# Performance work log

Measured on AMD Instinct MI355X. Metric: run time of the kernel, lower is better.

The kernel has to match this reference:

```python
import jax, jax.numpy as jnp
import numpy as np

B, LQ, LKV = 8, 512, 512
D, H, DH, FF = 1024, 16, 64, 4096
CH, CHID = 16, 32  # AttentionBiasMLP channels
EPS_LOG = 1e-6
EPS_LN = 1e-6


def _ln(x, g, b):
    mu = jnp.mean(x, axis=-1, keepdims=True)
    var = jnp.var(x, axis=-1, keepdims=True)
    return (x - mu) * jax.lax.rsqrt(var + EPS_LN) * g + b


def setup_inputs() -> dict:
    key = jax.random.key(0)
    ks = jax.random.split(key, 24)
    s = 0.02
    inp = {
        "q": jax.random.normal(ks[0], (B, LQ, D), jnp.float32),
        "kv": jax.random.normal(ks[1], (B, LKV, D), jnp.float32),
        "attn_map": jax.random.uniform(ks[2], (B, CH, LQ + 1, LKV + 1), jnp.float32),
        # attention projections (torch Linear: y = x @ W.T + b)
        "Wq": jax.random.normal(ks[3], (D, D)) * s, "bq": jnp.zeros((D,)),
        "Wk": jax.random.normal(ks[4], (D, D)) * s, "bk": jnp.zeros((D,)),
        "Wv": jax.random.normal(ks[5], (D, D)) * s, "bv": jnp.zeros((D,)),
        "Wm": jax.random.normal(ks[6], (D, D)) * s, "bm": jnp.zeros((D,)),
        # AttentionBiasMLP 1x1 convs: weight [out_ch, in_ch]
        "Wc1": jax.random.normal(ks[7], (CHID, CH)) * s, "bc1": jnp.zeros((CHID,)),
        "Wc2": jax.random.normal(ks[8], (CH, CHID)) * s, "bc2": jnp.zeros((CH,)),
        # FFN: Linear(D,FF) -> ReLU -> Linear(FF,D)
        "Wf1": jax.random.normal(ks[9], (FF, D)) * s, "bf1": jnp.zeros((FF,)),
        "Wf2": jax.random.normal(ks[10], (D, FF)) * s, "bf2": jnp.zeros((D,)),
        # LayerNorms
        "g1": jnp.ones((D,)), "b1": jnp.zeros((D,)),
        "g2": jnp.ones((D,)), "b2": jnp.zeros((D,)),
    }
    return inp


def _forward(q, kv, attn_map, Wq, bq, Wk, bk, Wv, bv, Wm, bm,
             Wc1, bc1, Wc2, bc2, Wf1, bf1, Wf2, bf2, g1, b1, g2, b2):
    # attention bias: log of cropped attn_map through 1x1-conv MLP with exact GELU
    log_map = jnp.log(attn_map[:, :, 1:, 1:] + EPS_LOG)               # [B,CH,LQ,LKV]
    h = jnp.einsum('bcqk,oc->boqk', log_map, Wc1) + bc1[None, :, None, None]
    h = jax.nn.gelu(h, approximate=False)
    attn_bias = jnp.einsum('bcqk,oc->boqk', h, Wc2) + bc2[None, :, None, None]

    # MHAtt: project, split heads
    qh = (q @ Wq.T + bq).reshape(B, LQ, H, DH).transpose(0, 2, 1, 3)   # [B,H,LQ,DH]
    kh = (kv @ Wk.T + bk).reshape(B, LKV, H, DH).transpose(0, 2, 1, 3)
    vh = (kv @ Wv.T + bv).reshape(B, LKV, H, DH).transpose(0, 2, 1, 3)

    scores = jnp.einsum('bhqd,bhkd->bhqk', qh, kh) / np.sqrt(DH).astype(np.float32)
    scores = scores + attn_bias
    att = jax.nn.softmax(scores, axis=-1)
    ctx = jnp.einsum('bhqk,bhkd->bhqd', att, vh)                       # [B,H,LQ,DH]
    ctx = ctx.transpose(0, 2, 1, 3).reshape(B, LQ, D)
    atted = ctx @ Wm.T + bm

    x = _ln(q + atted, g1, b1)
    ffn = jax.nn.relu(x @ Wf1.T + bf1) @ Wf2.T + bf2
    x = _ln(x + ffn, g2, b2)
    return x


def reference(q, kv, attn_map, Wq, bq, Wk, bk, Wv, bv, Wm, bm,
              Wc1, bc1, Wc2, bc2, Wf1, bf1, Wf2, bf2, g1, b1, g2, b2):
    return _forward(q, kv, attn_map, Wq, bq, Wk, bk, Wv, bv, Wm, bm,
                    Wc1, bc1, Wc2, bc2, Wf1, bf1, Wf2, bf2, g1, b1, g2, b2)
```

## Files before the change

### kernel.cpp

```cpp
#include <hip/hip_runtime.h>
#include <hip/hip_bf16.h>

typedef __bf16 bf16_t;
typedef __bf16 bf16x4_t __attribute__((ext_vector_type(4)));
typedef __bf16 bf16x8_t __attribute__((ext_vector_type(8)));
typedef float  f32x4_t  __attribute__((ext_vector_type(4)));

#define B_   8
#define LQ_  512
#define LKV_ 512
#define D_   1024
#define H_   16
#define DH_  64
#define FF_  4096

__device__ __forceinline__ f32x4_t mfma16(bf16x8_t a, bf16x8_t b, f32x4_t c) {
    return __builtin_amdgcn_mfma_f32_16x16x32_bf16(a, b, c, 0, 0, 0);
}

__device__ __forceinline__ void gload_lds16(const bf16_t* g, bf16_t* l) {
    __builtin_amdgcn_global_load_lds(
        (const __attribute__((address_space(1))) void*)g,
        (__attribute__((address_space(3))) void*)l, 16, 0, 0);
}

__device__ __forceinline__ int xcd_swz(int pid, int nwg) {
    return (pid & 7) * (nwg >> 3) + (pid >> 3);
}

__device__ __forceinline__ float gelu_fast(float h) {
    const float e = exp2f(h * -2.45546696f);
    return h * __builtin_amdgcn_rcpf(1.f + e);
}

__global__ __launch_bounds__(256)
void cvt_all_kernel(const float* __restrict__ q,  const float* __restrict__ kv,
                    const float* __restrict__ Wq, const float* __restrict__ Wk,
                    const float* __restrict__ Wv, const float* __restrict__ Wm,
                    const float* __restrict__ Wf1,const float* __restrict__ Wf2,
                    bf16_t* __restrict__ dq, bf16_t* __restrict__ dW,
                    bf16_t* __restrict__ dF) {
    const int i = blockIdx.x * 256 + threadIdx.x;
    const float* s; bf16_t* d; int j;
    if (i < 1048576)      { s = q;   d = dq;           j = i; }
    else if (i < 2097152) { s = kv;  d = dq + 4194304; j = i - 1048576; }
    else if (i < 2359296) { s = Wq;  d = dW;           j = i - 2097152; }
    else if (i < 2621440) { s = Wk;  d = dW + 1048576; j = i - 2359296; }
    else if (i < 2883584) { s = Wv;  d = dW + 2097152; j = i - 2621440; }
    else if (i < 3145728) { s = Wm;  d = dW + 3145728; j = i - 2883584; }
    else if (i < 4194304) { s = Wf1; d = dF;           j = i - 3145728; }
    else                  { s = Wf2; d = dF + 4194304; j = i - 4194304; }
    const float4 v = ((const float4*)s)[j];
    bf16x4_t o;
    o[0] = (bf16_t)v.x; o[1] = (bf16_t)v.y; o[2] = (bf16_t)v.z; o[3] = (bf16_t)v.w;
    ((bf16x4_t*)d)[j] = o;
}

__global__ __launch_bounds__(256)
void pack3_kernel(const float* __restrict__ a, const float* __restrict__ b,
                  const float* __restrict__ c, float* __restrict__ o) {
    const int i = blockIdx.x * 256 + threadIdx.x;
    o[i] = a[i]; o[1024 + i] = b[i]; o[2048 + i] = c[i];
}

__global__ __launch_bounds__(256)
void bias_mlp_mfma(const float* __restrict__ amap,
                   const float* __restrict__ Wc1, const float* __restrict__ bc1,
                   const float* __restrict__ Wc2, const float* __restrict__ bc2,
                   bf16_t* __restrict__ biasb) {
    __shared__ __align__(16) char lds[4][8192];
    const int t = threadIdx.x, lane = t & 63, w = t >> 6;
    const int l15 = lane & 15, lg = lane >> 4;
    char* Xs = lds[w];
    char* Hs = lds[w] + 3072;

    bf16x8_t b1f[2], b2f;
    f32x4_t bc1v[2];
#pragma unroll
    for (int ot = 0; ot < 2; ot++) {
        bf16x8_t v;
#pragma unroll
        for (int i = 0; i < 8; i++) {
            const int kk = (lg * 8 + i) & 15;
            const float wv = Wc1[(ot * 16 + l15) * 16 + kk] * 0.69314718055994531f;
            v[i] = (lg < 2) ? (bf16_t)wv : (bf16_t)0.f;
        }
        b1f[ot] = v;
        const float bb = bc1[ot * 16 + l15];
        bc1v[ot] = f32x4_t{bb, bb, bb, bb};
    }
    {
        bf16x8_t v;
#pragma unroll
        for (int i = 0; i < 8; i++) v[i] = (bf16_t)Wc2[l15 * 32 + lg * 8 + i];
        b2f = v;
    }
    const float bc2s = bc2[l15];
    const f32x4_t cinit2 = f32x4_t{bc2s, bc2s, bc2s, bc2s};

    const int posb = (blockIdx.x * 4 + w) * 64;
    const int b  = posb >> 18;
    const int q  = (posb >> 9) & 511;
    const int k0 = posb & 511;

    const float* src = amap + (size_t)(b * 16) * 263169 + (size_t)(q + 1) * 513 + (k0 + 1 + lane);
    bf16_t xr[16];
#pragma unroll
    for (int c = 0; c < 16; c++) {
        const float v = src[(size_t)c * 263169];
        xr[c] = (bf16_t)__log2f(v + 1e-6f);
    }
    *(bf16x8_t*)(Xs + lane * 48)      = *(bf16x8_t*)&xr[0];
    *(bf16x8_t*)(Xs + lane * 48 + 16) = *(bf16x8_t*)&xr[8];

    const int lgm16 = (lg & 1) * 16;
    f32x4_t h1[4][2];
#pragma unroll
    for (int p = 0; p < 4; p++) {
        const bf16x8_t a1 = *(const bf16x8_t*)(Xs + (p * 16 + l15) * 48 + lgm16);
#pragma unroll
        for (int ot = 0; ot < 2; ot++)
            h1[p][ot] = mfma16(a1, b1f[ot], bc1v[ot]);
    }

#pragma unroll
    for (int p = 0; p < 4; p++)
#pragma unroll
        for (int ot = 0; ot < 2; ot++)
#pragma unroll
            for (int r = 0; r < 4; r++) {
                const float g = gelu_fast(h1[p][ot][r]);
                *(bf16_t*)(Hs + (p * 16 + lg * 4 + r) * 80 + (ot * 16 + l15) * 2) = (bf16_t)g;
            }

    const size_t obase = ((size_t)(b * 16 + l15) * 512 + q) * 512 + k0;
#pragma unroll
    for (int p = 0; p < 4; p++) {
        const bf16x8_t a2 = *(const bf16x8_t*)(Hs + (p * 16 + l15) * 80 + lg * 16);
        const f32x4_t o2 = mfma16(a2, b2f, cinit2);
        bf16x4_t ov;
#pragma unroll
        for (int r = 0; r < 4; r++) ov[r] = (bf16_t)o2[r];
        *(bf16x4_t*)&biasb[obase + p * 16 + lg * 4] = ov;
    }
}

template <int EPI, bool SPLIT>
__global__ __launch_bounds__(256)
void gemm_bt(const bf16_t* __restrict__ A, const bf16_t* __restrict__ A2,
             const bf16_t* __restrict__ Bw,
             const float* __restrict__ bias, float* __restrict__ Cf,
             bf16_t* __restrict__ Cb, int M, int N, int Klen, int lda) {
    __shared__ __align__(16) bf16_t As[2][128 * 32];
    __shared__ __align__(16) bf16_t Bs[2][128 * 32];
    const int t = threadIdx.x, lane = t & 63, w = t >> 6;
    const int wr = w >> 1, wc = w & 1;
    const int ntn = N >> 7;
    const int nwg = (M >> 7) * ntn;
    const int wg  = xcd_swz((int)blockIdx.x, nwg);
    const int gsz = 8 * ntn;
    const int gid = wg / gsz;
    const int rem = wg - gid * gsz;
    const int tm  = gid * 8 + (rem & 7);
    const int tn  = rem >> 3;
    const int l15 = lane & 15, lg = lane >> 4;
    const int ks = SPLIT ? blockIdx.y : 0;
    const int koff = SPLIT ? ks * Klen : 0;
    if (EPI == 3 && tn >= 8) A = A2;

    const int c0_ = t;
    const int c1_ = t + 256;
    const int r0 = c0_ >> 2, k0 = c0_ & 3;
    const int r1 = c1_ >> 2, k1 = c1_ & 3;
    const int b0 = (w * 64) * 8;
    const int b1 = (256 + w * 64) * 8;
    const bf16_t* Abase0 = A  + (size_t)(tm * 128 + r0) * lda + koff + k0 * 8;
    const bf16_t* Abase1 = A  + (size_t)(tm * 128 + r1) * lda + koff + k1 * 8;
    const bf16_t* Bbase0 = Bw + (size_t)(tn * 128 + r0) * lda + koff + k0 * 8;
    const bf16_t* Bbase1 = Bw + (size_t)(tn * 128 + r1) * lda + koff + k1 * 8;

    f32x4_t acc[4][4];
#pragma unroll
    for (int i = 0; i < 4; i++)
#pragma unroll
        for (int j = 0; j < 4; j++) acc[i][j] = f32x4_t{0.f, 0.f, 0.f, 0.f};

    const int nk = Klen >> 5;

    gload_lds16(Abase0, &As[0][b0]);
    gload_lds16(Abase1, &As[0][b1]);
    gload_lds16(Bbase0, &Bs[0][b0]);
    gload_lds16(Bbase1, &Bs[0][b1]);
    asm volatile("s_waitcnt vmcnt(0)" ::: "memory");
    __syncthreads();

    int cur = 0;
    for (int kt = 0; kt < nk; ++kt) {
        if (kt + 1 < nk) {
            const int ko = (kt + 1) * 32;
            gload_lds16(Abase0 + ko, &As[cur ^ 1][b0]);
            gload_lds16(Abase1 + ko, &As[cur ^ 1][b1]);
            gload_lds16(Bbase0 + ko, &Bs[cur ^ 1][b0]);
            gload_lds16(Bbase1 + ko, &Bs[cur ^ 1][b1]);
        }

        const bf16_t* Ac = As[cur];
        const bf16_t* Bc = Bs[cur];
        bf16x8_t af[4], bfv[4];
#pragma unroll
        for (int mt = 0; mt < 4; mt++)
            af[mt] = *(const bf16x8_t*)&Ac[(wr * 64 + mt * 16 + l15) * 32 + lg * 8];
#pragma unroll
        for (int nt = 0; nt < 4; nt++)
            bfv[nt] = *(const bf16x8_t*)&Bc[(wc * 64 + nt * 16 + l15) * 32 + lg * 8];
#pragma unroll
        for (int mt = 0; mt < 4; mt++)
#pragma unroll
            for (int nt = 0; nt < 4; nt++)
                acc[mt][nt] = mfma16(af[mt], bfv[nt], acc[mt][nt]);

        if (kt + 1 < nk) {
            asm volatile("s_waitcnt vmcnt(0)" ::: "memory");
            __syncthreads();
            cur ^= 1;
        }
    }

#pragma unroll
    for (int nt = 0; nt < 4; nt++) {
        const int col = tn * 128 + wc * 64 + nt * 16 + l15;
        float bv = bias[col];
        if (SPLIT && ks != 0) bv = 0.f;
#pragma unroll
        for (int mt = 0; mt < 4; mt++) {
#pragma unroll
            for (int r = 0; r < 4; r++) {
                const int row = tm * 128 + wr * 64 + mt * 16 + lg * 4 + r;
                float v = acc[mt][nt][r] + bv;
                if (EPI == 2) v = fmaxf(v, 0.f);
                if (EPI == 3 && tn < 8) v *= 0.125f;
                if (EPI == 0) Cf[(size_t)ks * M * N + (size_t)row * N + col] = v;
                else if (EPI == 3)
                    Cb[(size_t)(col >> 10) * 4194304 + (size_t)row * 1024 + (col & 1023)] = (bf16_t)v;
                else Cb[(size_t)row * N + col] = (bf16_t)v;
            }
        }
    }
}

__global__ __launch_bounds__(256)
void attn_kernel(const bf16_t* __restrict__ Qp, const bf16_t* __restrict__ Kp,
                 const bf16_t* __restrict__ Vp, const bf16_t* __restrict__ biasb,
                 bf16_t* __restrict__ ctx) {
    __shared__ __align__(16) bf16_t Qs[64 * 64];
    __shared__ __align__(16) bf16_t Ks[64 * 64];
    __shared__ __align__(16) bf16_t Vts[64 * 64];
    __shared__ __align__(16) bf16_t Ps[64 * 64];
    __shared__ __align__(16) bf16_t Bbs[64 * 64];

    const int bid = xcd_swz((int)blockIdx.x, 1024);
    const int qt = bid & 7, h = (bid >> 3) & 15, b = bid >> 7;
    const int t = threadIdx.x, lane = t & 63, w = t >> 6;
    const int l15 = lane & 15, lg = lane >> 4;

#pragma unroll
    for (int i = 0; i < 2; i++) {
        const int c = t + i * 256;
        const int row = c >> 3, cg = c & 7;
        const uint4 v = *(const uint4*)&Qp[(((size_t)(b * LQ_ + qt * 64 + row)) * H_ + h) * DH_ + cg * 8];
        *(uint4*)((char*)Qs + row * 128 + ((cg ^ (row & 7)) << 4)) = v;
    }

    f32x4_t oacc[4];
#pragma unroll
    for (int i = 0; i < 4; i++) oacc[i] = f32x4_t{0.f, 0.f, 0.f, 0.f};
    float mrow[4] = {-1e30f, -1e30f, -1e30f, -1e30f};
    float lrow[4] = {0.f, 0.f, 0.f, 0.f};

    const bf16_t* bias_tile = biasb + ((size_t)(b * H_ + h) * LQ_ + qt * 64) * LKV_;

    for (int kt = 0; kt < 8; ++kt) {
        __syncthreads();
#pragma unroll
        for (int i = 0; i < 2; i++) {
            const int c = t + i * 256;
            const int row = c >> 3, cg = c & 7;
            const uint4 v = *(const uint4*)&Kp[(((size_t)(b * LKV_ + kt * 64 + row)) * H_ + h) * DH_ + cg * 8];
            *(uint4*)((char*)Ks + row * 128 + ((cg ^ (row & 7)) << 4)) = v;
        }
#pragma unroll
        for (int i = 0; i < 2; i++) {
            const int c = t + i * 256;
            const int row = c >> 3, cg = c & 7;
            const uint4 bv4 = *(const uint4*)&bias_tile[(size_t)row * LKV_ + kt * 64 + cg * 8];
            *(uint4*)&Bbs[row * 64 + cg * 8] = bv4;
        }
#pragma unroll
        for (int i = 0; i < 2; i++) {
            const int c = t + i * 256;
            const int k = c >> 3, dg = c & 7;
            const bf16x8_t vv = *(const bf16x8_t*)&Vp[(((size_t)(b * LKV_ + kt * 64 + k)) * H_ + h) * DH_ + dg * 8];
#pragma unroll
            for (int j = 0; j < 8; j++) {
                const int d = dg * 8 + j;
                *(bf16_t*)((char*)Vts + d * 128 + ((((k * 2) >> 4) ^ (d & 7)) << 4) + ((k * 2) & 15)) = vv[j];
            }
        }
        __syncthreads();

        f32x4_t sacc[4];
#pragma unroll
        for (int i = 0; i < 4; i++) sacc[i] = f32x4_t{0.f, 0.f, 0.f, 0.f};
        bf16x8_t aq[2];
        {
            const int rowq = w * 16 + l15;
#pragma unroll
            for (int kc = 0; kc < 2; kc++)
                aq[kc] = *(const bf16x8_t*)((const char*)Qs + rowq * 128 + (((kc * 4 + lg) ^ (rowq & 7)) << 4));
        }
#pragma unroll
        for (int nt = 0; nt < 4; nt++) {
            const int rowk = nt * 16 + l15;
#pragma unroll
            for (int kc = 0; kc < 2; kc++) {
                const bf16x8_t bk = *(const bf16x8_t*)((const char*)Ks + rowk * 128 + (((kc * 4 + lg) ^ (rowk & 7)) << 4));
                sacc[nt] = mfma16(aq[kc], bk, sacc[nt]);
            }
        }

        float esc[4];
#pragma unroll
        for (int r = 0; r < 4; r++) {
            const int qr = w * 16 + lg * 4 + r;
            float mx = -1e30f;
#pragma unroll
            for (int nt = 0; nt < 4; nt++) {
                const float bvv = (float)Bbs[qr * 64 + nt * 16 + l15];
                const float v = sacc[nt][r] + bvv;
                sacc[nt][r] = v;
                mx = fmaxf(mx, v);
            }
#pragma unroll
            for (int msk = 8; msk >= 1; msk >>= 1) mx = fmaxf(mx, __shfl_xor(mx, msk));
            const float mnew = fmaxf(mrow[r], mx);
            esc[r] = __expf(mrow[r] - mnew);
            mrow[r] = mnew;
            float rs = 0.f;
#pragma unroll
            for (int nt = 0; nt < 4; nt++) {
                const float p = __expf(sacc[nt][r] - mnew);
                sacc[nt][r] = p;
                rs += p;
            }
#pragma unroll
            for (int msk = 8; msk >= 1; msk >>= 1) rs += __shfl_xor(rs, msk);
            lrow[r] = lrow[r] * esc[r] + rs;
        }

#pragma unroll
        for (int r = 0; r < 4; r++) {
            const int prow = w * 16 + lg * 4 + r;
#pragma unroll
            for (int nt = 0; nt < 4; nt++) {
                const int pc2 = (nt * 16 + l15) * 2;
                *(bf16_t*)((char*)Ps + prow * 128 + (((pc2 >> 4) ^ (prow & 7)) << 4) + (pc2 & 15)) =
                    (bf16_t)sacc[nt][r];
            }
        }
        asm volatile("s_waitcnt lgkmcnt(0)" ::: "memory");
        __builtin_amdgcn_sched_barrier(0);

#pragma unroll
        for (int dt = 0; dt < 4; dt++)
#pragma unroll
            for (int r = 0; r < 4; r++) oacc[dt][r] *= esc[r];

        bf16x8_t pa[2];
        {
            const int rowp = w * 16 + l15;
#pragma unroll
            for (int kc = 0; kc < 2; kc++)
                pa[kc] = *(const bf16x8_t*)((const char*)Ps + rowp * 128 + (((kc * 4 + lg) ^ (rowp & 7)) << 4));
        }
#pragma unroll
        for (int dt = 0; dt < 4; dt++) {
            const int rowv = dt * 16 + l15;
#pragma unroll
            for (int kc = 0; kc < 2; kc++) {
                const bf16x8_t bv = *(const bf16x8_t*)((const char*)Vts + rowv * 128 + (((kc * 4 + lg) ^ (rowv & 7)) << 4));
                oacc[dt] = mfma16(pa[kc], bv, oacc[dt]);
            }
        }
    }

    float inv[4];
#pragma unroll
    for (int r = 0; r < 4; r++) inv[r] = __builtin_amdgcn_rcpf(lrow[r]);
#pragma unroll
    for (int dt = 0; dt < 4; dt++) {
#pragma unroll
        for (int r = 0; r < 4; r++) {
            const float v = oacc[dt][r] * inv[r];
            const int q = qt * 64 + w * 16 + lg * 4 + r;
            const int d = dt * 16 + l15;
            ctx[(((size_t)(b * LQ_ + q)) * H_ + h) * DH_ + d] = (bf16_t)v;
        }
    }
}

__global__ __launch_bounds__(256)
void add_ln3_kernel(const float* __restrict__ X, const float* __restrict__ Y0,
                    const float* __restrict__ Y1,
                    const float* __restrict__ g, const float* __restrict__ be,
                    float* __restrict__ of, bf16_t* __restrict__ ob) {
    const int row = blockIdx.x, t = threadIdx.x;
    const float4 xv = ((const float4*)(X + (size_t)row * 1024))[t];
    const float4 y0 = ((const float4*)(Y0 + (size_t)row * 1024))[t];
    const float4 y1 = ((const float4*)(Y1 + (size_t)row * 1024))[t];
    float v[4] = {xv.x + y0.x + y1.x, xv.y + y0.y + y1.y,
                  xv.z + y0.z + y1.z, xv.w + y0.w + y1.w};
    float s = v[0] + v[1] + v[2] + v[3];
    float s2 = v[0] * v[0] + v[1] * v[1] + v[2] * v[2] + v[3] * v[3];
#pragma unroll
    for (int m = 32; m >= 1; m >>= 1) { s += __shfl_xor(s, m); s2 += __shfl_xor(s2, m); }
    __shared__ float red[8];
    const int w = t >> 6, lane = t & 63;
    if (lane == 0) { red[w] = s; red[4 + w] = s2; }
    __syncthreads();
    s = red[0] + red[1] + red[2] + red[3];
    s2 = red[4] + red[5] + red[6] + red[7];
    const float mu = s * (1.f / 1024.f);
    const float var = s2 * (1.f / 1024.f) - mu * mu;
    const float rstd = rsqrtf(var + 1e-6f);
    const float4 gv = ((const float4*)g)[t];
    const float4 bv = ((const float4*)be)[t];
    float o[4];
    o[0] = (v[0] - mu) * rstd * gv.x + bv.x;
    o[1] = (v[1] - mu) * rstd * gv.y + bv.y;
    o[2] = (v[2] - mu) * rstd * gv.z + bv.z;
    o[3] = (v[3] - mu) * rstd * gv.w + bv.w;
    ((float4*)(of + (size_t)row * 1024))[t] = make_float4(o[0], o[1], o[2], o[3]);
    if (ob) {
        bf16x4_t qo;
        qo[0] = (bf16_t)o[0]; qo[1] = (bf16_t)o[1]; qo[2] = (bf16_t)o[2]; qo[3] = (bf16_t)o[3];
        ((bf16x4_t*)(ob + (size_t)row * 1024))[t] = qo;
    }
}

extern "C" void kernel_launch(void* const* d_in, const int* in_sizes, int n_in,
                              void* d_out, int out_size, void* d_ws, size_t ws_size,
                              hipStream_t stream) {
    (void)in_sizes; (void)n_in; (void)out_size; (void)ws_size;
    const float* q    = (const float*)d_in[0];
    const float* kv   = (const float*)d_in[1];
    const float* amap = (const float*)d_in[2];
    const float* Wq = (const float*)d_in[3];  const float* bQ = (const float*)d_in[4];
    const float* Wk = (const float*)d_in[5];  const float* bK = (const float*)d_in[6];
    const float* Wv = (const float*)d_in[7];  const float* bV = (const float*)d_in[8];
    const float* Wm = (const float*)d_in[9];  const float* bM = (const float*)d_in[10];
    const float* Wc1 = (const float*)d_in[11]; const float* bc1 = (const float*)d_in[12];
    const float* Wc2 = (const float*)d_in[13]; const float* bc2 = (const float*)d_in[14];
    const float* Wf1 = (const float*)d_in[15]; const float* bf1 = (const float*)d_in[16];
    const float* Wf2 = (const float*)d_in[17]; const float* bf2 = (const float*)d_in[18];
    const float* g1 = (const float*)d_in[19]; const float* b1 = (const float*)d_in[20];
    const float* g2 = (const float*)d_in[21]; const float* b2 = (const float*)d_in[22];

    char* w = (char*)d_ws;
    bf16_t* biasb = (bf16_t*)(w);
    float*  p0    = (float*)(w);
    float*  p1    = (float*)(w + 16777216);
    bf16_t* hb    = (bf16_t*)(w);
    float*  f0    = (float*)(w + 33554432);
    float*  f1    = (float*)(w + 50331648);
    bf16_t* qb   = (bf16_t*)(w + 67108864);
    bf16_t* kvb  = (bf16_t*)(w + 75497472);
    bf16_t* Qp   = (bf16_t*)(w + 83886080);
    bf16_t* Kp   = (bf16_t*)(w + 92274688);
    bf16_t* Vp   = (bf16_t*)(w + 100663296);
    bf16_t* Wqkvb = (bf16_t*)(w + 109051904);
    bf16_t* Wmb  = (bf16_t*)(w + 115343360);
    bf16_t* Wf1b = (bf16_t*)(w + 117440512);
    bf16_t* Wf2b = (bf16_t*)(w + 125829120);
    float*  bqkv = (float*)(w + 134217728);
    bf16_t* ctx = qb;
    float*  xf  = (float*)Qp;
    bf16_t* xb  = Vp;
    (void)Wmb; (void)Wf2b; (void)kvb;

    dim3 blk(256);
    cvt_all_kernel<<<20480, blk, 0, stream>>>(q, kv, Wq, Wk, Wv, Wm, Wf1, Wf2,
                                              qb, Wqkvb, Wf1b);
    pack3_kernel<<<4, blk, 0, stream>>>(bQ, bK, bV, bqkv);

    bias_mlp_mfma<<<8192, blk, 0, stream>>>(amap, Wc1, bc1, Wc2, bc2, biasb);

    gemm_bt<3, false><<<768, blk, 0, stream>>>(qb, kvb, Wqkvb, bqkv, nullptr, Qp,
                                               4096, 3072, 1024, 1024);

    attn_kernel<<<1024, blk, 0, stream>>>(Qp, Kp, Vp, biasb, ctx);

    gemm_bt<0, true><<<dim3(256, 2), blk, 0, stream>>>(ctx, nullptr, Wmb, bM, p0, nullptr,
                                                       4096, 1024, 512, 1024);
    add_ln3_kernel<<<4096, blk, 0, stream>>>(q, p0, p1, g1, b1, xf, xb);

    gemm_bt<2, false><<<1024, blk, 0, stream>>>(xb, nullptr, Wf1b, bf1, nullptr, hb,
                                                4096, 4096, 1024, 1024);
    gemm_bt<0, true><<<dim3(256, 2), blk, 0, stream>>>(hb, nullptr, Wf2b, bf2, f0, nullptr,
                                                       4096, 1024, 2048, 4096);
    add_ln3_kernel<<<4096, blk, 0, stream>>>(xf, f0, f1, g2, b2, (float*)d_out, nullptr);
}
```

Measured before the change: 332.8 us.

## Triple-buffer GEMM LDS pipeline, store split-K partials as bf16, hoist Q fragments

The GEMM mainloop moves from double to triple buffering of LDS tiles. Loads run two k-steps ahead, with a partial vmcnt wait and one barrier per iteration, to hide more global-load latency. Split-K partial outputs are written as bf16 instead of fp32, which halves partial-sum traffic into the add+LayerNorm kernels but loses precision in the residual path. In attention, the Q MFMA fragments are loaded once before the KV loop instead of on every tile. The added LDS per GEMM block may reduce occupancy.

```diff
diff --git a/kernel.cpp b/kernel.cpp
--- a/kernel.cpp
+++ b/kernel.cpp
@@ -149,10 +149,10 @@
 __global__ __launch_bounds__(256)
 void gemm_bt(const bf16_t* __restrict__ A, const bf16_t* __restrict__ A2,
              const bf16_t* __restrict__ Bw,
-             const float* __restrict__ bias, float* __restrict__ Cf,
+             const float* __restrict__ bias,
              bf16_t* __restrict__ Cb, int M, int N, int Klen, int lda) {
-    __shared__ __align__(16) bf16_t As[2][128 * 32];
-    __shared__ __align__(16) bf16_t Bs[2][128 * 32];
+    __shared__ __align__(16) bf16_t As[3][128 * 32];
+    __shared__ __align__(16) bf16_t Bs[3][128 * 32];
     const int t = threadIdx.x, lane = t & 63, w = t >> 6;
     const int wr = w >> 1, wc = w & 1;
     const int ntn = N >> 7;
@@ -168,10 +168,8 @@
     const int koff = SPLIT ? ks * Klen : 0;
     if (EPI == 3 && tn >= 8) A = A2;
 
-    const int c0_ = t;
-    const int c1_ = t + 256;
-    const int r0 = c0_ >> 2, k0 = c0_ & 3;
-    const int r1 = c1_ >> 2, k1 = c1_ & 3;
+    const int r0 = t >> 2,          k0 = t & 3;
+    const int r1 = (t + 256) >> 2,  k1 = t & 3;
     const int b0 = (w * 64) * 8;
     const int b1 = (256 + w * 64) * 8;
     const bf16_t* Abase0 = A  + (size_t)(tm * 128 + r0) * lda + koff + k0 * 8;
@@ -187,21 +185,26 @@
 
     const int nk = Klen >> 5;
 
-    gload_lds16(Abase0, &As[0][b0]);
-    gload_lds16(Abase1, &As[0][b1]);
-    gload_lds16(Bbase0, &Bs[0][b0]);
-    gload_lds16(Bbase1, &Bs[0][b1]);
-    asm volatile("s_waitcnt vmcnt(0)" ::: "memory");
-    __syncthreads();
+#define STAGE(KT, S)                                    \
+    do {                                                \
+        const int _ko = (KT) * 32;                      \
+        gload_lds16(Abase0 + _ko, &As[(S)][b0]);        \
+        gload_lds16(Abase1 + _ko, &As[(S)][b1]);        \
+        gload_lds16(Bbase0 + _ko, &Bs[(S)][b0]);        \
+        gload_lds16(Bbase1 + _ko, &Bs[(S)][b1]);        \
+    } while (0)
+
+    STAGE(0, 0);
+    STAGE(1, 1);
 
     int cur = 0;
     for (int kt = 0; kt < nk; ++kt) {
-        if (kt + 1 < nk) {
-            const int ko = (kt + 1) * 32;
-            gload_lds16(Abase0 + ko, &As[cur ^ 1][b0]);
-            gload_lds16(Abase1 + ko, &As[cur ^ 1][b1]);
-            gload_lds16(Bbase0 + ko, &Bs[cur ^ 1][b0]);
-            gload_lds16(Bbase1 + ko, &Bs[cur ^ 1][b1]);
+        if (kt + 1 < nk) { asm volatile("s_waitcnt vmcnt(4)" ::: "memory"); }
+        else             { asm volatile("s_waitcnt vmcnt(0)" ::: "memory"); }
+        __syncthreads();
+        if (kt + 2 < nk) {
+            const int s2 = cur >= 1 ? cur - 1 : cur + 2;
+            STAGE(kt + 2, s2);
         }
 
         const bf16_t* Ac = As[cur];
@@ -219,12 +222,9 @@
             for (int nt = 0; nt < 4; nt++)
                 acc[mt][nt] = mfma16(af[mt], bfv[nt], acc[mt][nt]);
 
-        if (kt + 1 < nk) {
-            asm volatile("s_waitcnt vmcnt(0)" ::: "memory");
-            __syncthreads();
-            cur ^= 1;
-        }
-    }
+        cur = cur < 2 ? cur + 1 : 0;
+    }
+#undef STAGE
 
 #pragma unroll
     for (int nt = 0; nt < 4; nt++) {
@@ -239,7 +239,8 @@
                 float v = acc[mt][nt][r] + bv;
                 if (EPI == 2) v = fmaxf(v, 0.f);
                 if (EPI == 3 && tn < 8) v *= 0.125f;
-                if (EPI == 0) Cf[(size_t)ks * M * N + (size_t)row * N + col] = v;
+                if (SPLIT)
+                    Cb[(size_t)ks * M * N + (size_t)row * N + col] = (bf16_t)v;
                 else if (EPI == 3)
                     Cb[(size_t)(col >> 10) * 4194304 + (size_t)row * 1024 + (col & 1023)] = (bf16_t)v;
                 else Cb[(size_t)row * N + col] = (bf16_t)v;
@@ -270,6 +271,15 @@
         const uint4 v = *(const uint4*)&Qp[(((size_t)(b * LQ_ + qt * 64 + row)) * H_ + h) * DH_ + cg * 8];
         *(uint4*)((char*)Qs + row * 128 + ((cg ^ (row & 7)) << 4)) = v;
     }
+    __syncthreads();
+
+    bf16x8_t aq[2];
+    {
+        const int rowq = w * 16 + l15;
+#pragma unroll
+        for (int kc = 0; kc < 2; kc++)
+            aq[kc] = *(const bf16x8_t*)((const char*)Qs + rowq * 128 + (((kc * 4 + lg) ^ (rowq & 7)) << 4));
+    }
 
     f32x4_t oacc[4];
 #pragma unroll
@@ -311,13 +321,6 @@
         f32x4_t sacc[4];
 #pragma unroll
         for (int i = 0; i < 4; i++) sacc[i] = f32x4_t{0.f, 0.f, 0.f, 0.f};
-        bf16x8_t aq[2];
-        {
-            const int rowq = w * 16 + l15;
-#pragma unroll
-            for (int kc = 0; kc < 2; kc++)
-                aq[kc] = *(const bf16x8_t*)((const char*)Qs + rowq * 128 + (((kc * 4 + lg) ^ (rowq & 7)) << 4));
-        }
 #pragma unroll
         for (int nt = 0; nt < 4; nt++) {
             const int rowk = nt * 16 + l15;
@@ -409,16 +412,16 @@
 }
 
 __global__ __launch_bounds__(256)
-void add_ln3_kernel(const float* __restrict__ X, const float* __restrict__ Y0,
-                    const float* __restrict__ Y1,
+void add_ln3_kernel(const float* __restrict__ X, const bf16_t* __restrict__ Y0,
+                    const bf16_t* __restrict__ Y1,
                     const float* __restrict__ g, const float* __restrict__ be,
                     float* __restrict__ of, bf16_t* __restrict__ ob) {
     const int row = blockIdx.x, t = threadIdx.x;
     const float4 xv = ((const float4*)(X + (size_t)row * 1024))[t];
-    const float4 y0 = ((const float4*)(Y0 + (size_t)row * 1024))[t];
-    const float4 y1 = ((const float4*)(Y1 + (size_t)row * 1024))[t];
-    float v[4] = {xv.x + y0.x + y1.x, xv.y + y0.y + y1.y,
-                  xv.z + y0.z + y1.z, xv.w + y0.w + y1.w};
+    const bf16x4_t y0 = ((const bf16x4_t*)(Y0 + (size_t)row * 1024))[t];
+    const bf16x4_t y1 = ((const bf16x4_t*)(Y1 + (size_t)row * 1024))[t];
+    float v[4] = {xv.x + (float)y0[0] + (float)y1[0], xv.y + (float)y0[1] + (float)y1[1],
+                  xv.z + (float)y0[2] + (float)y1[2], xv.w + (float)y0[3] + (float)y1[3]};
     float s = v[0] + v[1] + v[2] + v[3];
     float s2 = v[0] * v[0] + v[1] * v[1] + v[2] * v[2] + v[3] * v[3];
 #pragma unroll
@@ -467,11 +470,11 @@
 
     char* w = (char*)d_ws;
     bf16_t* biasb = (bf16_t*)(w);
-    float*  p0    = (float*)(w);
-    float*  p1    = (float*)(w + 16777216);
+    bf16_t* p0    = (bf16_t*)(w);
+    bf16_t* p1    = (bf16_t*)(w + 8388608);
     bf16_t* hb    = (bf16_t*)(w);
-    float*  f0    = (float*)(w + 33554432);
-    float*  f1    = (float*)(w + 50331648);
+    bf16_t* f0    = (bf16_t*)(w + 33554432);
+    bf16_t* f1    = (bf16_t*)(w + 41943040);
     bf16_t* qb   = (bf16_t*)(w + 67108864);
     bf16_t* kvb  = (bf16_t*)(w + 75497472);
     bf16_t* Qp   = (bf16_t*)(w + 83886080);
@@ -485,7 +488,6 @@
     bf16_t* ctx = qb;
     float*  xf  = (float*)Qp;
     bf16_t* xb  = Vp;
-    (void)Wmb; (void)Wf2b; (void)kvb;
 
     dim3 blk(256);
     cvt_all_kernel<<<20480, blk, 0, stream>>>(q, kv, Wq, Wk, Wv, Wm, Wf1, Wf2,
@@ -494,18 +496,18 @@
 
     bias_mlp_mfma<<<8192, blk, 0, stream>>>(amap, Wc1, bc1, Wc2, bc2, biasb);
 
-    gemm_bt<3, false><<<768, blk, 0, stream>>>(qb, kvb, Wqkvb, bqkv, nullptr, Qp,
+    gemm_bt<3, false><<<768, blk, 0, stream>>>(qb, kvb, Wqkvb, bqkv, Qp,
                                                4096, 3072, 1024, 1024);
 
     attn_kernel<<<1024, blk, 0, stream>>>(Qp, Kp, Vp, biasb, ctx);
 
-    gemm_bt<0, true><<<dim3(256, 2), blk, 0, stream>>>(ctx, nullptr, Wmb, bM, p0, nullptr,
+    gemm_bt<0, true><<<dim3(256, 2), blk, 0, stream>>>(ctx, nullptr, Wmb, bM, p0,
                                                        4096, 1024, 512, 1024);
     add_ln3_kernel<<<4096, blk, 0, stream>>>(q, p0, p1, g1, b1, xf, xb);
 
-    gemm_bt<2, false><<<1024, blk, 0, stream>>>(xb, nullptr, Wf1b, bf1, nullptr, hb,
+    gemm_bt<2, false><<<1024, blk, 0, stream>>>(xb, nullptr, Wf1b, bf1, hb,
                                                 4096, 4096, 1024, 1024);
-    gemm_bt<0, true><<<dim3(256, 2), blk, 0, stream>>>(hb, nullptr, Wf2b, bf2, f0, nullptr,
+    gemm_bt<0, true><<<dim3(256, 2), blk, 0, stream>>>(hb, nullptr, Wf2b, bf2, f0,
                                                        4096, 1024, 2048, 4096);
     add_ln3_kernel<<<4096, blk, 0, stream>>>(xf, f0, f1, g2, b2, (float*)d_out, nullptr);
 }
```

After: 329.9 us. Within noise of the previous version (-0.9%).
